# Optimization experiments

Measured on AMD Instinct MI355X. Metric: run time of the kernel, lower is better.

The kernel has to match this reference:

```python
import jax, jax.numpy as jnp
import numpy as np

HEADS1, HID, LSTM_H, OUT = 4, 64, 32, 2
NEG_SLOPE = 0.2
EPS = 1e-16


def gat_layer(x, src, dst, W, att_src, att_dst, bias, heads, out_ch):
    """PyG GATConv (concat=True, add_self_loops handled by caller)."""
    N = x.shape[0]
    h = (x @ W).reshape(N, heads, out_ch)                 # [N, H, C]
    a_s = jnp.sum(h * att_src, axis=-1)                    # [N, H]
    a_d = jnp.sum(h * att_dst, axis=-1)                    # [N, H]
    e = jax.nn.leaky_relu(a_s[src] + a_d[dst], NEG_SLOPE)  # [E, H]
    m = jax.ops.segment_max(e, dst, num_segments=N)        # scatter-softmax (stable)
    e = jnp.exp(e - jax.lax.stop_gradient(m)[dst])
    denom = jax.ops.segment_sum(e, dst, num_segments=N)
    alpha = e / (denom[dst] + EPS)                         # [E, H]
    msg = h[src] * alpha[..., None]                        # [E, H, C]
    out = jax.ops.segment_sum(msg, dst, num_segments=N)    # [N, H, C]
    return out.reshape(N, heads * out_ch) + bias


def lstm_last(seq, W_ih, W_hh, b_ih, b_hh, hidden):
    """Single-layer batch_first LSTM; returns last-step hidden state. Gate order i,f,g,o (torch)."""
    B = seq.shape[0]
    xT = jnp.transpose(seq, (1, 0, 2))  # [T, B, F]
    b = b_ih + b_hh

    def step(carry, xt):
        h, c = carry
        z = xt @ W_ih.T + h @ W_hh.T + b  # [B, 4H]
        i, f, g, o = jnp.split(z, 4, axis=-1)
        c = jax.nn.sigmoid(f) * c + jax.nn.sigmoid(i) * jnp.tanh(g)
        h = jax.nn.sigmoid(o) * jnp.tanh(c)
        return (h, c), None

    h0 = jnp.zeros((B, hidden), seq.dtype)
    (h, _), _ = jax.lax.scan(step, (h0, h0), xT)
    return h


def setup_inputs() -> dict:
    key = jax.random.key(0)
    ks = jax.random.split(key, 20)
    N, E, IN, T = 50000, 800000, 128, 50
    s = lambda k, shp: jax.random.normal(k, shp, jnp.float32) * 0.05
    inp = {
        "x": jax.random.normal(ks[0], (N, IN), jnp.float32),
        "edge_index": jax.random.randint(ks[1], (2, E), 0, N, jnp.int32),
        "sequences": jax.random.normal(ks[2], (N, T, 3), jnp.float32),
        # GATConv 1: in=128 -> 64 per head, 4 heads
        "W1": s(ks[3], (IN, HEADS1 * HID)),
        "att_src1": s(ks[4], (HEADS1, HID)),
        "att_dst1": s(ks[5], (HEADS1, HID)),
        "bias1": jnp.zeros((HEADS1 * HID,), jnp.float32),
        # GATConv 2: in=256 -> 64, 1 head
        "W2": s(ks[6], (HEADS1 * HID, HID)),
        "att_src2": s(ks[7], (1, HID)),
        "att_dst2": s(ks[8], (1, HID)),
        "bias2": jnp.zeros((HID,), jnp.float32),
        # LSTM(input_size=3, hidden_size=32)
        "W_ih": s(ks[9], (4 * LSTM_H, 3)),
        "W_hh": s(ks[10], (4 * LSTM_H, LSTM_H)),
        "b_ih": jnp.zeros((4 * LSTM_H,), jnp.float32),
        "b_hh": jnp.zeros((4 * LSTM_H,), jnp.float32),
        # fusion MLP: (64+32) -> 64 -> 2
        "Wf1": s(ks[11], (HID + LSTM_H, HID)),
        "bf1": jnp.zeros((HID,), jnp.float32),
        "Wf2": s(ks[12], (HID, OUT)),
        "bf2": jnp.zeros((OUT,), jnp.float32),
    }
    return inp


def reference(x, edge_index, sequences, W1, att_src1, att_dst1, bias1,
              W2, att_src2, att_dst2, bias2, W_ih, W_hh, b_ih, b_hh,
              Wf1, bf1, Wf2, bf2):
    N = x.shape[0]
    # PyG GATConv default add_self_loops=True
    loops = jnp.arange(N, dtype=edge_index.dtype)
    src = jnp.concatenate([edge_index[0], loops])
    dst = jnp.concatenate([edge_index[1], loops])

    g = jax.nn.elu(gat_layer(x, src, dst, W1, att_src1, att_dst1, bias1, HEADS1, HID))
    # dropout is identity in eval mode
    g = gat_layer(g, src, dst, W2, att_src2, att_dst2, bias2, 1, HID)  # [N, 64]

    t = lstm_last(sequences, W_ih, W_hh, b_ih, b_hh, LSTM_H)           # [N, 32]

    combined = jnp.concatenate([g, t], axis=1)
    h = jax.nn.relu(combined @ Wf1 + bf1)
    return h @ Wf2 + bf2
```

## Files before the change

### kernel.cpp

```cpp
#include <hip/hip_runtime.h>
#include <math.h>

#define HEADS1 4
#define HID 64
#define LSTM_H 32
#define IN_F 128
#define T_STEPS 50
#define NEG_SLOPE 0.2f
#define EPS_A 1e-16f

typedef __attribute__((ext_vector_type(8))) short short8;
typedef __attribute__((ext_vector_type(4))) float floatx4;
typedef __attribute__((ext_vector_type(4))) unsigned uint32x4;

__device__ __forceinline__ float frcp(float x) {
    float r;
    asm("v_rcp_f32 %0, %1" : "=v"(r) : "v"(x));
    return r;
}
__device__ __forceinline__ float sigf(float x) { return frcp(1.0f + __expf(-x)); }
__device__ __forceinline__ float tanhfast(float x) {
    float e = __expf(2.0f * x);
    return 1.0f - 2.0f * frcp(e + 1.0f);
}
__device__ __forceinline__ unsigned short f2bf(float f) {
    unsigned u = __float_as_uint(f);
    unsigned r = (u + 0x7FFFu + ((u >> 16) & 1u)) >> 16;
    return (unsigned short)r;
}
__device__ __forceinline__ float bf2f(unsigned short s) {
    return __uint_as_float(((unsigned)s) << 16);
}
__device__ __forceinline__ unsigned cvt_pk_bf16(float a, float b) {
    unsigned r;
    asm("v_cvt_pk_bf16_f32 %0, %1, %2" : "=v"(r) : "v"(a), "v"(b));
    return r;
}
__device__ __forceinline__ float lo16f(unsigned p) { return __uint_as_float(p << 16); }
__device__ __forceinline__ float hi16f(unsigned p) { return __uint_as_float(p & 0xffff0000u); }
__device__ __forceinline__ short8 bc8(uint32x4 v) { return __builtin_bit_cast(short8, v); }

template <int KK>
__global__ void prep_wt(const float* __restrict__ W, unsigned short* __restrict__ th,
                        unsigned short* __restrict__ tl, int total, int NC) {
    int i = blockIdx.x * 256 + threadIdx.x;
    if (i >= total) return;
    int n = i / KK, k = i - n * KK;
    float v = W[k * NC + n];
    unsigned short h = f2bf(v);
    th[i] = h;
    tl[i] = f2bf(v - bf2f(h));
}

template <int K, int NC>
__global__ __launch_bounds__(256)
void gemm_mfma(const float* __restrict__ A, const unsigned short* __restrict__ Bth,
               const unsigned short* __restrict__ Btl, float* __restrict__ C, int M) {
    __shared__ float sA[128][44];
    __shared__ unsigned short sBh[64][40];
    __shared__ unsigned short sBl[64][40];
    const int tid = threadIdx.x;
    const int wave = tid >> 6, lane = tid & 63;
    const int wr = wave >> 1, wc = wave & 1;
    const int row0 = blockIdx.x * 128;
    const int col0 = blockIdx.y * 64;
    const int l15 = lane & 15, l4 = lane >> 4;

    floatx4 acc[4][2];
#pragma unroll
    for (int rb = 0; rb < 4; rb++)
#pragma unroll
        for (int cb = 0; cb < 2; cb++) acc[rb][cb] = (floatx4){0.f, 0.f, 0.f, 0.f};

    for (int k0 = 0; k0 < K; k0 += 32) {
        __syncthreads();
#pragma unroll
        for (int q = 0; q < 4; q++) {
            int idx = q * 256 + tid;
            int row = idx >> 3, seg = idx & 7;
            int gr = row0 + row;
            float4 v = (gr < M) ? *(const float4*)&A[(size_t)gr * K + k0 + seg * 4]
                                : make_float4(0.f, 0.f, 0.f, 0.f);
            *(float4*)&sA[row][seg * 4] = v;
        }
        {
            int col = tid >> 2, seg = tid & 3;
            size_t gb = (size_t)(col0 + col) * K + k0 + seg * 8;
            *(short8*)&sBh[col][seg * 8] = *(const short8*)&Bth[gb];
            *(short8*)&sBl[col][seg * 8] = *(const short8*)&Btl[gb];
        }
        __syncthreads();

        short8 bh0 = *(const short8*)&sBh[wc * 32 + 0 + l15][l4 * 8];
        short8 bl0 = *(const short8*)&sBl[wc * 32 + 0 + l15][l4 * 8];
        short8 bh1 = *(const short8*)&sBh[wc * 32 + 16 + l15][l4 * 8];
        short8 bl1 = *(const short8*)&sBl[wc * 32 + 16 + l15][l4 * 8];

#pragma unroll
        for (int rb = 0; rb < 4; rb++) {
            int row = wr * 64 + rb * 16 + l15;
            floatx4 a0 = *(const floatx4*)&sA[row][l4 * 8 + 0];
            floatx4 a1 = *(const floatx4*)&sA[row][l4 * 8 + 4];
            unsigned p0 = cvt_pk_bf16(a0[0], a0[1]);
            unsigned p1 = cvt_pk_bf16(a0[2], a0[3]);
            unsigned p2 = cvt_pk_bf16(a1[0], a1[1]);
            unsigned p3 = cvt_pk_bf16(a1[2], a1[3]);
            uint32x4 hp = {p0, p1, p2, p3};
            short8 Ah = bc8(hp);
            unsigned q0 = cvt_pk_bf16(a0[0] - lo16f(p0), a0[1] - hi16f(p0));
            unsigned q1 = cvt_pk_bf16(a0[2] - lo16f(p1), a0[3] - hi16f(p1));
            unsigned q2 = cvt_pk_bf16(a1[0] - lo16f(p2), a1[1] - hi16f(p2));
            unsigned q3 = cvt_pk_bf16(a1[2] - lo16f(p3), a1[3] - hi16f(p3));
            uint32x4 lp = {q0, q1, q2, q3};
            short8 Al = bc8(lp);

            acc[rb][0] = __builtin_amdgcn_mfma_f32_16x16x32_bf16(Ah, bh0, acc[rb][0], 0, 0, 0);
            acc[rb][0] = __builtin_amdgcn_mfma_f32_16x16x32_bf16(Ah, bl0, acc[rb][0], 0, 0, 0);
            acc[rb][0] = __builtin_amdgcn_mfma_f32_16x16x32_bf16(Al, bh0, acc[rb][0], 0, 0, 0);
            acc[rb][1] = __builtin_amdgcn_mfma_f32_16x16x32_bf16(Ah, bh1, acc[rb][1], 0, 0, 0);
            acc[rb][1] = __builtin_amdgcn_mfma_f32_16x16x32_bf16(Ah, bl1, acc[rb][1], 0, 0, 0);
            acc[rb][1] = __builtin_amdgcn_mfma_f32_16x16x32_bf16(Al, bh1, acc[rb][1], 0, 0, 0);
        }
    }

#pragma unroll
    for (int rb = 0; rb < 4; rb++)
#pragma unroll
        for (int cb = 0; cb < 2; cb++)
#pragma unroll
            for (int q = 0; q < 4; q++) {
                int row = row0 + wr * 64 + rb * 16 + l4 * 4 + q;
                int col = col0 + wc * 32 + cb * 16 + l15;
                if (row < M) C[(size_t)row * NC + col] = acc[rb][cb][q];
            }
}

__global__ void att_scores(const float* __restrict__ h, const float* __restrict__ att_s,
                           const float* __restrict__ att_d, float* __restrict__ as_,
                           float* __restrict__ ad_, int NH, int Hmask) {
    int i = blockIdx.x * blockDim.x + threadIdx.x;
    if (i >= NH) return;
    int hh = i & Hmask;
    const float* row = h + (size_t)i * HID;
    float s = 0.0f, d = 0.0f;
#pragma unroll 8
    for (int c = 0; c < HID; c++) {
        float v = row[c];
        s += v * att_s[hh * HID + c];
        d += v * att_d[hh * HID + c];
    }
    as_[i] = s;
    ad_[i] = d;
}

__global__ void count_deg(const int* __restrict__ dsts, int E, int ET, int* __restrict__ cnt) {
    int e = blockIdx.x * blockDim.x + threadIdx.x;
    if (e >= ET) return;
    int d = (e < E) ? dsts[e] : (e - E);
    atomicAdd(&cnt[d], 1);
}

__global__ void scan1(const int* __restrict__ cnt, int* __restrict__ rowp,
                      int* __restrict__ bsum, int N) {
    __shared__ int tmp[256];
    int i = blockIdx.x * 256 + threadIdx.x;
    int v = (i < N) ? cnt[i] : 0;
    tmp[threadIdx.x] = v;
    __syncthreads();
    for (int off = 1; off < 256; off <<= 1) {
        int t = (threadIdx.x >= (unsigned)off) ? tmp[threadIdx.x - off] : 0;
        __syncthreads();
        tmp[threadIdx.x] += t;
        __syncthreads();
    }
    if (i < N) rowp[i] = tmp[threadIdx.x] - v;
    if (threadIdx.x == 255) bsum[blockIdx.x] = tmp[255];
}

__global__ void scan2(int* __restrict__ bsum, int nb) {
    __shared__ int tmp[256];
    int v = (threadIdx.x < (unsigned)nb) ? bsum[threadIdx.x] : 0;
    tmp[threadIdx.x] = v;
    __syncthreads();
    for (int off = 1; off < 256; off <<= 1) {
        int t = (threadIdx.x >= (unsigned)off) ? tmp[threadIdx.x - off] : 0;
        __syncthreads();
        tmp[threadIdx.x] += t;
        __syncthreads();
    }
    if (threadIdx.x < (unsigned)nb) bsum[threadIdx.x] = tmp[threadIdx.x] - v;
}

__global__ void scan3(int* __restrict__ rowp, const int* __restrict__ bsum, int N, int ET) {
    int i = blockIdx.x * 256 + threadIdx.x;
    if (i < N) rowp[i] += bsum[blockIdx.x];
    if (i == 0) rowp[N] = ET;
}

__global__ void scatter_edges(const int* __restrict__ dsts, int E, int ET,
                              const int* __restrict__ rowp, int* __restrict__ cursor,
                              int* __restrict__ eid) {
    int e = blockIdx.x * blockDim.x + threadIdx.x;
    if (e >= ET) return;
    int d = (e < E) ? dsts[e] : (e - E);
    int pos = atomicAdd(&cursor[d], 1);
    eid[rowp[d] + pos] = e;
}

__global__ __launch_bounds__(256)
void gat_agg4_sp(const int* __restrict__ srcs, int E,
                 const int* __restrict__ rowp, const int* __restrict__ eid,
                 const float* __restrict__ as_, const float* __restrict__ ad_,
                 const float* __restrict__ hfeat, const float* __restrict__ bias,
                 float* __restrict__ g, int N) {
    __shared__ float s_alpha[4][64][4];
    const int wave = threadIdx.x >> 6;
    const int lane = threadIdx.x & 63;
    const int head = lane >> 4;
    const int dst = blockIdx.x * 4 + wave;
    if (dst >= N) return;
    const int start = rowp[dst], end = rowp[dst + 1];
    const float4 adv = ((const float4*)ad_)[dst];
    const float4* h4 = (const float4*)hfeat;

    float4 dsum = make_float4(0.f, 0.f, 0.f, 0.f);
    float4 acc  = make_float4(0.f, 0.f, 0.f, 0.f);

    for (int i0 = start; i0 < end; i0 += 64) {
        int cnt = min(64, end - i0);
        int i = i0 + lane;
        int s = 0;
        if (i < end) {
            int e = eid[i];
            s = (e < E) ? srcs[e] : (e - E);
            float4 a = ((const float4*)as_)[s];
            float tx, ex;
            tx = a.x + adv.x; tx = (tx > 0.f) ? tx : NEG_SLOPE * tx; ex = __expf(tx);
            dsum.x += ex; s_alpha[wave][lane][0] = ex;
            tx = a.y + adv.y; tx = (tx > 0.f) ? tx : NEG_SLOPE * tx; ex = __expf(tx);
            dsum.y += ex; s_alpha[wave][lane][1] = ex;
            tx = a.z + adv.z; tx = (tx > 0.f) ? tx : NEG_SLOPE * tx; ex = __expf(tx);
            dsum.z += ex; s_alpha[wave][lane][2] = ex;
            tx = a.w + adv.w; tx = (tx > 0.f) ? tx : NEG_SLOPE * tx; ex = __expf(tx);
            dsum.w += ex; s_alpha[wave][lane][3] = ex;
        }
        __builtin_amdgcn_wave_barrier();
#pragma unroll 4
        for (int k = 0; k < cnt; k++) {
            float a_k = s_alpha[wave][k][head];
            int   s_k = __shfl(s, k);
            float4 hv = h4[(size_t)s_k * 64 + lane];
            acc.x += a_k * hv.x; acc.y += a_k * hv.y;
            acc.z += a_k * hv.z; acc.w += a_k * hv.w;
        }
        __builtin_amdgcn_wave_barrier();
    }
#pragma unroll
    for (int mk = 32; mk >= 1; mk >>= 1) {
        dsum.x += __shfl_xor(dsum.x, mk);
        dsum.y += __shfl_xor(dsum.y, mk);
        dsum.z += __shfl_xor(dsum.z, mk);
        dsum.w += __shfl_xor(dsum.w, mk);
    }
    float den = (head == 0) ? dsum.x : (head == 1) ? dsum.y : (head == 2) ? dsum.z : dsum.w;
    float inv = 1.0f / (den + EPS_A);
    float4 b4 = ((const float4*)bias)[lane];
    float4 r;
    r.x = acc.x * inv + b4.x; r.x = (r.x > 0.f) ? r.x : __expf(r.x) - 1.f;
    r.y = acc.y * inv + b4.y; r.y = (r.y > 0.f) ? r.y : __expf(r.y) - 1.f;
    r.z = acc.z * inv + b4.z; r.z = (r.z > 0.f) ? r.z : __expf(r.z) - 1.f;
    r.w = acc.w * inv + b4.w; r.w = (r.w > 0.f) ? r.w : __expf(r.w) - 1.f;
    ((float4*)g)[(size_t)dst * 64 + lane] = r;
}

__global__ __launch_bounds__(256)
void gat_agg1_sp(const int* __restrict__ srcs, int E,
                 const int* __restrict__ rowp, const int* __restrict__ eid,
                 const float* __restrict__ as_, const float* __restrict__ ad_,
                 const float* __restrict__ hfeat, const float* __restrict__ bias,
                 float* __restrict__ g, int N) {
    __shared__ float s_alpha[4][64];
    const int wave = threadIdx.x >> 6;
    const int lane = threadIdx.x & 63;
    const int dst = blockIdx.x * 4 + wave;
    if (dst >= N) return;
    const int start = rowp[dst], end = rowp[dst + 1];
    const float adv = ad_[dst];

    float dsum = 0.0f, acc = 0.0f;
    for (int i0 = start; i0 < end; i0 += 64) {
        int cnt = min(64, end - i0);
        int i = i0 + lane;
        int s = 0;
        if (i < end) {
            int e = eid[i];
            s = (e < E) ? srcs[e] : (e - E);
            float t = as_[s] + adv;
            t = (t > 0.f) ? t : NEG_SLOPE * t;
            float ex = __expf(t);
            dsum += ex;
            s_alpha[wave][lane] = ex;
        }
        __builtin_amdgcn_wave_barrier();
#pragma unroll 4
        for (int k = 0; k < cnt; k++) {
            float a_k = s_alpha[wave][k];
            int   s_k = __shfl(s, k);
            acc += a_k * hfeat[(size_t)s_k * 64 + lane];
        }
        __builtin_amdgcn_wave_barrier();
    }
#pragma unroll
    for (int mk = 32; mk >= 1; mk >>= 1) dsum += __shfl_xor(dsum, mk);
    g[(size_t)dst * 64 + lane] = acc / (dsum + EPS_A) + bias[lane];
}

__global__ void prep_wsplit(const float* __restrict__ Wih, const float* __restrict__ Whh,
                            const float* __restrict__ bih, const float* __restrict__ bhh,
                            uint32x4* __restrict__ wsp) {
    const int tid = threadIdx.x;
    const int kk = tid >> 7, sub = (tid >> 6) & 1, lane = tid & 63;
    const int grp = lane >> 4, col = lane & 15;
    const int krow = grp * 8;
    const int n = (sub + kk * 2) * 16 + col;
    float w[8];
    *(float4*)&w[0] = *(const float4*)&Whh[n * 32 + krow + 0];
    *(float4*)&w[4] = *(const float4*)&Whh[n * 32 + krow + 4];
    unsigned hi[8], lo[8];
#pragma unroll
    for (int j = 0; j < 8; j++) {
        unsigned short hs = f2bf(w[j]);
        hi[j] = hs;
        lo[j] = f2bf(w[j] - bf2f(hs));
    }
    uint32x4 BH = {hi[0] | (hi[1] << 16), hi[2] | (hi[3] << 16),
                   hi[4] | (hi[5] << 16), hi[6] | (hi[7] << 16)};
    uint32x4 BL = {lo[0] | (lo[1] << 16), lo[2] | (lo[3] << 16),
                   lo[4] | (lo[5] << 16), lo[6] | (lo[7] << 16)};
    float wi0 = Wih[n * 3 + 0], wi1 = Wih[n * 3 + 1], wi2 = Wih[n * 3 + 2];
    float bb = bih[n] + bhh[n];
    unsigned h0 = f2bf(wi0), h1 = f2bf(wi1), h2 = f2bf(wi2), hb = f2bf(bb);
    uint32x4 B2 = {0u, 0u, 0u, 0u};
    if (grp == 0) {
        unsigned bl_ = f2bf(bb - bf2f((unsigned short)hb));
        B2[0] = h0 | (h1 << 16); B2[1] = h2 | (hb << 16);
        B2[2] = h0 | (h1 << 16); B2[3] = h2 | (bl_ << 16);
    } else if (grp == 1) {
        unsigned l0 = f2bf(wi0 - bf2f((unsigned short)h0));
        unsigned l1 = f2bf(wi1 - bf2f((unsigned short)h1));
        unsigned l2 = f2bf(wi2 - bf2f((unsigned short)h2));
        B2[0] = l0 | (l1 << 16); B2[1] = l2;
    }
    wsp[((kk * 3 + 0) * 2 + sub) * 64 + lane] = B2;
    wsp[((kk * 3 + 1) * 2 + sub) * 64 + lane] = BH;
    wsp[((kk * 3 + 2) * 2 + sub) * 64 + lane] = BL;
}

__global__ __launch_bounds__(512)
__attribute__((amdgpu_waves_per_eu(2, 4)))
void lstm_mfma(const float* __restrict__ seq, const uint32x4* __restrict__ wsp,
               float* __restrict__ t_out, int N) {
    __shared__ float s_seq[9600];
    __shared__ float s_h[4][2][16][36];

    const int tid  = threadIdx.x;
    const int wave = tid >> 6, lane = tid & 63;
    const int pair = wave >> 1, sub = wave & 1;
    const int grp  = lane >> 4, col = lane & 15;
    const int node0 = blockIdx.x * 64 + pair * 16;

    {
        const size_t base  = (size_t)blockIdx.x * 9600;
        const size_t limit = (size_t)N * 150;
        for (int i = tid * 4; i < 9600; i += 512 * 4) {
            size_t g = base + i;
            float4 v;
            if (g + 3 < limit) {
                v = *(const float4*)&seq[g];
            } else {
                v.x = (g + 0 < limit) ? seq[g + 0] : 0.0f;
                v.y = (g + 1 < limit) ? seq[g + 1] : 0.0f;
                v.z = (g + 2 < limit) ? seq[g + 2] : 0.0f;
                v.w = (g + 3 < limit) ? seq[g + 3] : 0.0f;
            }
            *(float4*)&s_seq[i] = v;
        }
    }

#define LF(KK, W) wsp[(((KK) * 3 + (W)) * 2 + sub) * 64 + lane]
    uint32x4 B2_0 = LF(0, 0), BH_0 = LF(0, 1), BL_0 = LF(0, 2);
    uint32x4 B2_1 = LF(1, 0), BH_1 = LF(1, 1), BL_1 = LF(1, 2);
    uint32x4 B2_2 = LF(2, 0), BH_2 = LF(2, 1), BL_2 = LF(2, 2);
    uint32x4 B2_3 = LF(3, 0), BH_3 = LF(3, 1), BL_3 = LF(3, 2);
#undef LF
    asm volatile("" : "+v"(B2_0), "+v"(BH_0), "+v"(BL_0),
                      "+v"(B2_1), "+v"(BH_1), "+v"(BL_1),
                      "+v"(B2_2), "+v"(BH_2), "+v"(BL_2),
                      "+v"(B2_3), "+v"(BH_3), "+v"(BL_3));

    for (int i = tid; i < 4 * 2 * 16 * 36; i += 512) ((float*)s_h)[i] = 0.0f;
    __syncthreads();

    float cst0 = 0.f, cst1 = 0.f, cst2 = 0.f, cst3 = 0.f;
    float hn0 = 0.f, hn1 = 0.f, hn2 = 0.f, hn3 = 0.f;
    const floatx4 zac = {0.f, 0.f, 0.f, 0.f};

    const bool g0 = (grp == 0);
    const float* xrow = &s_seq[(pair * 16 + col) * 150];

#pragma unroll 1
    for (int t = 0; t < T_STEPS; t++) {
        float xv0 = xrow[t * 3 + 0];
        float xv1 = xrow[t * 3 + 1];
        float xv2 = xrow[t * 3 + 2];

        unsigned w0 = cvt_pk_bf16(xv0, xv1);
        unsigned w1 = cvt_pk_bf16(xv2, g0 ? 1.0f : 0.0f);
        float e0 = xv0 - lo16f(w0);
        float e1 = xv1 - hi16f(w0);
        float e2 = xv2 - lo16f(w1);
        unsigned w2 = g0 ? cvt_pk_bf16(e0, e1) : 0u;
        unsigned w3 = g0 ? cvt_pk_bf16(e2, 1.0f) : 0u;
        uint32x4 a2p = {w0, w1, w2, w3};
        short8 A2 = bc8(a2p);

        const float* hr = &s_h[pair][(t + 1) & 1][col][grp * 8];
        floatx4 h0 = *(const floatx4*)&hr[0];
        floatx4 h1 = *(const floatx4*)&hr[4];
        unsigned p0 = cvt_pk_bf16(h0[0], h0[1]);
        unsigned p1 = cvt_pk_bf16(h0[2], h0[3]);
        unsigned p2 = cvt_pk_bf16(h1[0], h1[1]);
        unsigned p3 = cvt_pk_bf16(h1[2], h1[3]);
        uint32x4 hip = {p0, p1, p2, p3};
        short8 Ahi = bc8(hip);
        unsigned q0 = cvt_pk_bf16(h0[0] - lo16f(p0), h0[1] - hi16f(p0));
        unsigned q1 = cvt_pk_bf16(h0[2] - lo16f(p1), h0[3] - hi16f(p1));
        unsigned q2 = cvt_pk_bf16(h1[0] - lo16f(p2), h1[1] - hi16f(p2));
        unsigned q3 = cvt_pk_bf16(h1[2] - lo16f(p3), h1[3] - hi16f(p3));
        uint32x4 lop = {q0, q1, q2, q3};
        short8 Alo = bc8(lop);

        floatx4 d0 = __builtin_amdgcn_mfma_f32_16x16x32_bf16(A2, bc8(B2_0), zac, 0, 0, 0);
        d0 = __builtin_amdgcn_mfma_f32_16x16x32_bf16(Alo, bc8(BH_0), d0, 0, 0, 0);
        d0 = __builtin_amdgcn_mfma_f32_16x16x32_bf16(Ahi, bc8(BL_0), d0, 0, 0, 0);
        d0 = __builtin_amdgcn_mfma_f32_16x16x32_bf16(Ahi, bc8(BH_0), d0, 0, 0, 0);
        floatx4 d1 = __builtin_amdgcn_mfma_f32_16x16x32_bf16(A2, bc8(B2_1), zac, 0, 0, 0);
        d1 = __builtin_amdgcn_mfma_f32_16x16x32_bf16(Alo, bc8(BH_1), d1, 0, 0, 0);
        d1 = __builtin_amdgcn_mfma_f32_16x16x32_bf16(Ahi, bc8(BL_1), d1, 0, 0, 0);
        d1 = __builtin_amdgcn_mfma_f32_16x16x32_bf16(Ahi, bc8(BH_1), d1, 0, 0, 0);
        floatx4 d2 = __builtin_amdgcn_mfma_f32_16x16x32_bf16(A2, bc8(B2_2), zac, 0, 0, 0);
        d2 = __builtin_amdgcn_mfma_f32_16x16x32_bf16(Alo, bc8(BH_2), d2, 0, 0, 0);
        d2 = __builtin_amdgcn_mfma_f32_16x16x32_bf16(Ahi, bc8(BL_2), d2, 0, 0, 0);
        d2 = __builtin_amdgcn_mfma_f32_16x16x32_bf16(Ahi, bc8(BH_2), d2, 0, 0, 0);
        floatx4 d3 = __builtin_amdgcn_mfma_f32_16x16x32_bf16(A2, bc8(B2_3), zac, 0, 0, 0);
        d3 = __builtin_amdgcn_mfma_f32_16x16x32_bf16(Alo, bc8(BH_3), d3, 0, 0, 0);
        d3 = __builtin_amdgcn_mfma_f32_16x16x32_bf16(Ahi, bc8(BL_3), d3, 0, 0, 0);
        d3 = __builtin_amdgcn_mfma_f32_16x16x32_bf16(Ahi, bc8(BH_3), d3, 0, 0, 0);

        {
            float ig, fg, gv, og;
            ig = sigf(d0[0]); fg = sigf(d1[0]); gv = tanhfast(d2[0]); og = sigf(d3[0]);
            cst0 = fg * cst0 + ig * gv; hn0 = og * tanhfast(cst0);
            ig = sigf(d0[1]); fg = sigf(d1[1]); gv = tanhfast(d2[1]); og = sigf(d3[1]);
            cst1 = fg * cst1 + ig * gv; hn1 = og * tanhfast(cst1);
            ig = sigf(d0[2]); fg = sigf(d1[2]); gv = tanhfast(d2[2]); og = sigf(d3[2]);
            cst2 = fg * cst2 + ig * gv; hn2 = og * tanhfast(cst2);
            ig = sigf(d0[3]); fg = sigf(d1[3]); gv = tanhfast(d2[3]); og = sigf(d3[3]);
            cst3 = fg * cst3 + ig * gv; hn3 = og * tanhfast(cst3);
        }

        float* hw = &s_h[pair][t & 1][4 * grp][sub * 16 + col];
        hw[0 * 36] = hn0; hw[1 * 36] = hn1; hw[2 * 36] = hn2; hw[3 * 36] = hn3;
        __syncthreads();
    }

    {
        int node = node0 + 4 * grp;
        const int c = sub * 16 + col;
        if (node + 0 < N) t_out[(size_t)(node + 0) * LSTM_H + c] = hn0;
        if (node + 1 < N) t_out[(size_t)(node + 1) * LSTM_H + c] = hn1;
        if (node + 2 < N) t_out[(size_t)(node + 2) * LSTM_H + c] = hn2;
        if (node + 3 < N) t_out[(size_t)(node + 3) * LSTM_H + c] = hn3;
    }
}

__global__ void fusion_kernel(const float* __restrict__ g2, const float* __restrict__ tt,
                              const float* __restrict__ Wf1, const float* __restrict__ bf1,
                              const float* __restrict__ Wf2, const float* __restrict__ bf2,
                              float* __restrict__ out, int N) {
    __shared__ float sW[96 * 64];
    __shared__ float sb1[64];
    __shared__ float sW2[128];
    for (int i = threadIdx.x; i < 96 * 64; i += 256) sW[i] = Wf1[i];
    if (threadIdx.x < 64) sb1[threadIdx.x] = bf1[threadIdx.x];
    if (threadIdx.x < 128) sW2[threadIdx.x] = Wf2[threadIdx.x];
    __syncthreads();
    const int wave = threadIdx.x >> 6;
    const int lane = threadIdx.x & 63;
    for (int n = blockIdx.x * 4 + wave; n < N; n += gridDim.x * 4) {
        const float* gn = g2 + (size_t)n * 64;
        const float* tn = tt + (size_t)n * 32;
        float acc = sb1[lane];
#pragma unroll 8
        for (int k = 0; k < 64; k++) acc += gn[k] * sW[k * 64 + lane];
#pragma unroll 8
        for (int k = 0; k < 32; k++) acc += tn[k] * sW[(64 + k) * 64 + lane];
        acc = fmaxf(acc, 0.0f);
        float o0 = acc * sW2[lane * 2 + 0];
        float o1 = acc * sW2[lane * 2 + 1];
#pragma unroll
        for (int mk = 32; mk >= 1; mk >>= 1) {
            o0 += __shfl_xor(o0, mk);
            o1 += __shfl_xor(o1, mk);
        }
        if (lane == 0) {
            out[(size_t)n * 2 + 0] = o0 + bf2[0];
            out[(size_t)n * 2 + 1] = o1 + bf2[1];
        }
    }
}

extern "C" void kernel_launch(void* const* d_in, const int* in_sizes, int n_in,
                              void* d_out, int out_size, void* d_ws, size_t ws_size,
                              hipStream_t stream) {
    const float* x      = (const float*)d_in[0];
    const int*   eidx   = (const int*)d_in[1];
    const float* seq    = (const float*)d_in[2];
    const float* W1     = (const float*)d_in[3];
    const float* att_s1 = (const float*)d_in[4];
    const float* att_d1 = (const float*)d_in[5];
    const float* bias1  = (const float*)d_in[6];
    const float* W2     = (const float*)d_in[7];
    const float* att_s2 = (const float*)d_in[8];
    const float* att_d2 = (const float*)d_in[9];
    const float* bias2  = (const float*)d_in[10];
    const float* Wih    = (const float*)d_in[11];
    const float* Whh    = (const float*)d_in[12];
    const float* bih    = (const float*)d_in[13];
    const float* bhh    = (const float*)d_in[14];
    const float* Wf1    = (const float*)d_in[15];
    const float* bf1    = (const float*)d_in[16];
    const float* Wf2    = (const float*)d_in[17];
    const float* bf2    = (const float*)d_in[18];
    float* out = (float*)d_out;

    const int N  = in_sizes[0] / IN_F;
    const int E  = in_sizes[1] / 2;
    const int ET = E + N;
    const int* srcs = eidx;
    const int* dsts = eidx + E;

    float* fws = (float*)d_ws;
    size_t o = 0;
    float* h1  = fws + o; o += (size_t)N * 256;
    float* g1  = fws + o; o += (size_t)N * 256;
    float* as1 = fws + o; o += (size_t)N * 4;
    float* ad1 = fws + o; o += (size_t)N * 4;
    int* cnt    = (int*)(fws + o);
    int* rowp   = cnt + N;
    int* cursor = rowp + N + 1;
    int* eid    = cursor + N;
    int* bsum   = eid + ET;
    uintptr_t wp_ = (uintptr_t)(bsum + 512);
    wp_ = (wp_ + 15) & ~(uintptr_t)15;
    uint32x4* wsp = (uint32x4*)wp_;
    unsigned short* w1h = (unsigned short*)(wsp + 1536);
    unsigned short* w1l = w1h + 32768;
    unsigned short* w2h = w1l + 32768;
    unsigned short* w2l = w2h + 16384;
    float* h2 = h1;
    float* g2 = h1 + (size_t)N * 64;
    float* tt = h1 + (size_t)N * 128;
    float* as2 = as1; float* ad2 = ad1;

    const int nTiles = (N + 255) / 256;
    dim3 blk(256);

    hipMemsetAsync(cnt, 0, (size_t)N * sizeof(int), stream);
    hipMemsetAsync(cursor, 0, (size_t)N * sizeof(int), stream);
    count_deg<<<(ET + 255) / 256, blk, 0, stream>>>(dsts, E, ET, cnt);
    scan1<<<nTiles, blk, 0, stream>>>(cnt, rowp, bsum, N);
    scan2<<<1, blk, 0, stream>>>(bsum, nTiles);
    scan3<<<(N + 256) / 256, blk, 0, stream>>>(rowp, bsum, N, ET);
    scatter_edges<<<(ET + 255) / 256, blk, 0, stream>>>(dsts, E, ET, rowp, cursor, eid);

    prep_wsplit<<<1, 512, 0, stream>>>(Wih, Whh, bih, bhh, wsp);
    prep_wt<128><<<(32768 + 255) / 256, blk, 0, stream>>>(W1, w1h, w1l, 32768, 256);
    prep_wt<256><<<(16384 + 255) / 256, blk, 0, stream>>>(W2, w2h, w2l, 16384, 64);

    gemm_mfma<128, 256><<<dim3((N + 127) / 128, 4), blk, 0, stream>>>(x, w1h, w1l, h1, N);
    att_scores<<<(N * 4 + 255) / 256, blk, 0, stream>>>(h1, att_s1, att_d1, as1, ad1, N * 4, 3);
    gat_agg4_sp<<<(N + 3) / 4, blk, 0, stream>>>(srcs, E, rowp, eid, as1, ad1, h1, bias1, g1, N);

    lstm_mfma<<<(N + 63) / 64, dim3(512), 0, stream>>>(seq, wsp, tt, N);

    gemm_mfma<256, 64><<<dim3((N + 127) / 128, 1), blk, 0, stream>>>(g1, w2h, w2l, h2, N);
    att_scores<<<(N + 255) / 256, blk, 0, stream>>>(h2, att_s2, att_d2, as2, ad2, N, 0);
    gat_agg1_sp<<<(N + 3) / 4, blk, 0, stream>>>(srcs, E, rowp, eid, as2, ad2, h2, bias2, g2, N);

    fusion_kernel<<<512, blk, 0, stream>>>(g2, tt, Wf1, bf1, Wf2, bf2, out, N);
}
```

Before: 731.4 us.

## Stream LSTM inputs directly from global memory with per-step register prefetch

Drops the 38 KB shared-memory staging of each block's input sequence. Each lane now loads its node's three features for the next timestep straight from global memory into registers, one step ahead, overlapping the load with the MFMA chain. The waves_per_eu attribute is also removed. Freeing LDS is meant to raise occupancy and remove the upfront bulk load and its barrier, at the cost of small strided global loads on the latency-critical recurrent loop.

```diff
diff --git a/kernel.cpp b/kernel.cpp
--- a/kernel.cpp
+++ b/kernel.cpp
@@ -357,10 +357,8 @@
 }
 
 __global__ __launch_bounds__(512)
-__attribute__((amdgpu_waves_per_eu(2, 4)))
 void lstm_mfma(const float* __restrict__ seq, const uint32x4* __restrict__ wsp,
                float* __restrict__ t_out, int N) {
-    __shared__ float s_seq[9600];
     __shared__ float s_h[4][2][16][36];
 
     const int tid  = threadIdx.x;
@@ -368,24 +366,6 @@
     const int pair = wave >> 1, sub = wave & 1;
     const int grp  = lane >> 4, col = lane & 15;
     const int node0 = blockIdx.x * 64 + pair * 16;
-
-    {
-        const size_t base  = (size_t)blockIdx.x * 9600;
-        const size_t limit = (size_t)N * 150;
-        for (int i = tid * 4; i < 9600; i += 512 * 4) {
-            size_t g = base + i;
-            float4 v;
-            if (g + 3 < limit) {
-                v = *(const float4*)&seq[g];
-            } else {
-                v.x = (g + 0 < limit) ? seq[g + 0] : 0.0f;
-                v.y = (g + 1 < limit) ? seq[g + 1] : 0.0f;
-                v.z = (g + 2 < limit) ? seq[g + 2] : 0.0f;
-                v.w = (g + 3 < limit) ? seq[g + 3] : 0.0f;
-            }
-            *(float4*)&s_seq[i] = v;
-        }
-    }
 
 #define LF(KK, W) wsp[(((KK) * 3 + (W)) * 2 + sub) * 64 + lane]
     uint32x4 B2_0 = LF(0, 0), BH_0 = LF(0, 1), BL_0 = LF(0, 2);
@@ -405,15 +385,17 @@
     float hn0 = 0.f, hn1 = 0.f, hn2 = 0.f, hn3 = 0.f;
     const floatx4 zac = {0.f, 0.f, 0.f, 0.f};
 
+    const int nodeX = node0 + col;
+    const bool vx = (nodeX < N) && (grp < 2);
     const bool g0 = (grp == 0);
-    const float* xrow = &s_seq[(pair * 16 + col) * 150];
+    const float* xp = seq + (size_t)nodeX * (T_STEPS * 3);
+
+    float xv0 = vx ? xp[0] : 0.0f;
+    float xv1 = vx ? xp[1] : 0.0f;
+    float xv2 = vx ? xp[2] : 0.0f;
 
 #pragma unroll 1
     for (int t = 0; t < T_STEPS; t++) {
-        float xv0 = xrow[t * 3 + 0];
-        float xv1 = xrow[t * 3 + 1];
-        float xv2 = xrow[t * 3 + 2];
-
         unsigned w0 = cvt_pk_bf16(xv0, xv1);
         unsigned w1 = cvt_pk_bf16(xv2, g0 ? 1.0f : 0.0f);
         float e0 = xv0 - lo16f(w0);
@@ -439,6 +421,13 @@
         unsigned q3 = cvt_pk_bf16(h1[2] - lo16f(p3), h1[3] - hi16f(p3));
         uint32x4 lop = {q0, q1, q2, q3};
         short8 Alo = bc8(lop);
+
+        {
+            int tn = (t + 1 < T_STEPS) ? (t + 1) : t;
+            xv0 = vx ? xp[tn * 3 + 0] : 0.0f;
+            xv1 = vx ? xp[tn * 3 + 1] : 0.0f;
+            xv2 = vx ? xp[tn * 3 + 2] : 0.0f;
+        }
 
         floatx4 d0 = __builtin_amdgcn_mfma_f32_16x16x32_bf16(A2, bc8(B2_0), zac, 0, 0, 0);
         d0 = __builtin_amdgcn_mfma_f32_16x16x32_bf16(Alo, bc8(BH_0), d0, 0, 0, 0);
```

Result: no change. 726.7 us (-0.6%).
